# Kernel tuning notes

Measured on AMD Instinct MI355X. Metric: run time of the kernel, lower is better.

## Reference

```python
import jax, jax.numpy as jnp
import numpy as np

N = 16384

def setup_inputs() -> dict:
    key = jax.random.key(0)
    k1, k2, k3 = jax.random.split(key, 3)
    risk = jax.random.normal(k1, (N,), dtype=jnp.float32)
    time = jax.random.uniform(k2, (N,), dtype=jnp.float32)
    event = jax.random.randint(k3, (N,), 0, 2).astype(jnp.float32)
    return {"risk": risk, "time": time, "event": event}

def reference(risk, time, event):
    theta = risk.reshape(-1)  # [n]
    # Risk-set mask: R[i, j] = 1.0 iff time[j] >= time[i]  (same as the torch double loop)
    R_mat = (time[None, :] >= time[:, None]).astype(theta.dtype)  # [n, n]
    exp_theta = jnp.exp(theta)  # [n]
    log_risk_set = jnp.log(R_mat @ exp_theta)  # [n]
    loss = -((theta - log_risk_set) * event).sum() / event.sum()
    return loss
```

## Files before the change

kernel.cpp:

```cpp
#include <hip/hip_runtime.h>

#define NR    16
#define LOCB  1024
#define CAP   1536
#define BLK   1024

__device__ __forceinline__ int keyof(float t) {
    int k = (int)(t * 16384.f);
    return k < 0 ? 0 : (k > 16383 ? 16383 : k);
}

__global__ __launch_bounds__(BLK)
void cox_one(const float* __restrict__ risk,
             const float* __restrict__ tm,
             const float* __restrict__ event,
             float* __restrict__ out, int n) {
    __shared__ float4 S4[CAP];
    __shared__ int    cnt[LOCB];
    __shared__ int    off[LOCB];
    __shared__ float  bsm[LOCB];
    __shared__ float2 TE[CAP];
    __shared__ float  wsc[16], wsc2[16], sn[16];
    __shared__ int    s_m;
    __shared__ float  s_gsuf, s_den;
    const int g    = blockIdx.x;
    const int tid  = threadIdx.x;
    const int lane = tid & 63;
    const int wave = tid >> 6;

    cnt[tid] = 0; bsm[tid] = 0.f;
    if (tid == 0) { s_m = 0; s_gsuf = 0.f; s_den = 0.f; }
    __syncthreads();

    const float4* tm4 = (const float4*)tm;
    const float4* rk4 = (const float4*)risk;
    const float4* ev4 = (const float4*)event;
    const int nq = n >> 2;
    float gsufp = 0.f, denp = 0.f;

    auto quad = [&](const float4 t4, const float4 r4, const float4 e4) {
        #pragma unroll
        for (int c = 0; c < 4; ++c) {
            const float t  = c == 0 ? t4.x : c == 1 ? t4.y : c == 2 ? t4.z : t4.w;
            const float rk = c == 0 ? r4.x : c == 1 ? r4.y : c == 2 ? r4.z : r4.w;
            const float ev = c == 0 ? e4.x : c == 1 ? e4.y : c == 2 ? e4.z : e4.w;
            const int   key = keyof(t);
            const int   r   = key >> 10;
            denp += ev;
            if (r >= g) {
                const float e = __expf(rk);
                if (r > g) {
                    gsufp += e;
                } else {
                    const int lbk = key & (LOCB - 1);
                    const int pos = atomicAdd(&s_m, 1);
                    S4[pos] = make_float4(t, e, rk, ev);
                    atomicAdd(&cnt[lbk], 1);
                    atomicAdd(&bsm[lbk], e);
                }
            }
        }
    };

    if (nq == 4 * BLK) {
        float4 T[4], R[4], E[4];
        #pragma unroll
        for (int it = 0; it < 4; ++it) {
            const int q = tid + it * BLK;
            T[it] = tm4[q]; R[it] = rk4[q]; E[it] = ev4[q];
        }
        #pragma unroll
        for (int it = 0; it < 4; ++it) quad(T[it], R[it], E[it]);
    } else {
        for (int q = tid; q < nq; q += BLK) quad(tm4[q], rk4[q], ev4[q]);
    }

    #pragma unroll
    for (int o = 32; o > 0; o >>= 1) {
        denp  += __shfl_down(denp, o);
        gsufp += __shfl_down(gsufp, o);
    }
    if (lane == 0) { atomicAdd(&s_den, denp); atomicAdd(&s_gsuf, gsufp); }
    __syncthreads();
    const int   m    = s_m;
    const float gsuf = s_gsuf;
    const float den  = s_den;

    {
        const int   c = cnt[tid];
        const float e = bsm[tid];
        int incl = c;
        #pragma unroll
        for (int o = 1; o < 64; o <<= 1) {
            const int tmp = __shfl_up(incl, o);
            if (lane >= o) incl += tmp;
        }
        float fincl = e;
        #pragma unroll
        for (int o = 1; o < 64; o <<= 1) {
            const float tmp = __shfl_down(fincl, o);
            if (lane + o < 64) fincl += tmp;
        }
        if (lane == 63) wsc[wave]  = (float)incl;
        if (lane == 0)  wsc2[wave] = fincl;
        __syncthreads();
        int croff = 0;
        for (int w = 0; w < wave; ++w) croff += (int)wsc[w];
        float crsuf = 0.f;
        for (int w = wave + 1; w < 16; ++w) crsuf += wsc2[w];
        off[tid] = croff + incl - c;
        bsm[tid] = crsuf + (fincl - e);
    }
    __syncthreads();

    for (int idx = tid; idx < m; idx += BLK) {
        const float4 v   = S4[idx];
        const int    lbk = keyof(v.x) & (LOCB - 1);
        const int    pos = atomicAdd(&off[lbk], 1);
        TE[pos] = make_float2(v.x, v.y);
    }
    __syncthreads();

    float num = 0.f;
    for (int idx = tid; idx < m; idx += BLK) {
        const float4 v     = S4[idx];
        const int    b     = keyof(v.x) & (LOCB - 1);
        const int    end   = off[b];
        const int    start = end - cnt[b];
        float corr = 0.f;
        for (int q = start; q < end; ++q) {
            const float2 te = TE[q];
            corr += (te.x >= v.x) ? te.y : 0.f;
        }
        num += (v.z - logf(gsuf + bsm[b] + corr)) * v.w;
    }

    #pragma unroll
    for (int o = 32; o > 0; o >>= 1) num += __shfl_down(num, o);
    if (lane == 0) sn[wave] = num;
    __syncthreads();
    if (tid == 0) {
        float tn = 0.f;
        #pragma unroll
        for (int w = 0; w < 16; ++w) tn += sn[w];
        atomicAdd(out, -tn / den);
    }
}

extern "C" void kernel_launch(void* const* d_in, const int* in_sizes, int n_in,
                              void* d_out, int out_size, void* d_ws, size_t ws_size,
                              hipStream_t stream) {
    const float* risk  = (const float*)d_in[0];
    const float* tm    = (const float*)d_in[1];
    const float* event = (const float*)d_in[2];
    float* out = (float*)d_out;
    const int n = in_sizes[0];

    cox_one<<<NR, BLK, 0, stream>>>(risk, tm, event, out, n);
}
```

Before: 63.85 us.

## Split Cox loss into a 64-block scatter pass and a 16-block solve pass

Adds a first kernel with 64 blocks that reads each input element once, computes exp, and scatters records into per-range, per-chunk staging buffers in workspace along with per-chunk counts, exp sums and event sums. The second kernel then has each of the 16 range blocks load only its own staged records plus the small count/sum arrays, replacing the old scheme where every block rescanned all N inputs. The aim is to spread the input pass across more CUs and cut redundant global reads and exp work. The cost is an extra kernel launch and a global round trip through workspace. The old single kernel remains as a fallback when n differs.

```diff
diff --git a/kernel.cpp b/kernel.cpp
--- a/kernel.cpp
+++ b/kernel.cpp
@@ -4,22 +4,70 @@
 #define LOCB  1024
 #define CAP   1536
 #define BLK   1024
+#define NB1   64
+#define B1T   256
+#define CHCAP 256
 
 __device__ __forceinline__ int keyof(float t) {
     int k = (int)(t * 16384.f);
     return k < 0 ? 0 : (k > 16383 ? 16383 : k);
 }
 
+
+
+__global__ __launch_bounds__(B1T)
+void cox_scatter(const float* __restrict__ risk, const float* __restrict__ tm,
+                 const float* __restrict__ event, float4* __restrict__ staged,
+                 int* __restrict__ cnts, float* __restrict__ sums,
+                 float* __restrict__ denw) {
+    __shared__ int   c16[NR];
+    __shared__ float s16[NR];
+    __shared__ float sden[B1T / 64];
+    const int b = blockIdx.x, tid = threadIdx.x;
+    if (tid < NR) { c16[tid] = 0; s16[tid] = 0.f; }
+    __syncthreads();
+
+    const int   i  = b * B1T + tid;
+    const float t  = tm[i];
+    const float rk = risk[i];
+    const float ev = event[i];
+    const int   key = keyof(t);
+    const int   r   = key >> 10;
+    const float e   = __expf(rk);
+    const int   pos = atomicAdd(&c16[r], 1);
+    staged[(r * NB1 + b) * CHCAP + pos] = make_float4(t, e, rk, ev);
+    atomicAdd(&s16[r], e);
+
+    float dp = ev;
+    #pragma unroll
+    for (int o = 32; o > 0; o >>= 1) dp += __shfl_down(dp, o);
+    const int lane = tid & 63, wv = tid >> 6;
+    if (lane == 0) sden[wv] = dp;
+    __syncthreads();
+
+    if (tid < NR) {
+        cnts[tid * NB1 + b] = c16[tid];
+        sums[tid * NB1 + b] = s16[tid];
+    }
+    if (tid == 0) {
+        float d = 0.f;
+        #pragma unroll
+        for (int w = 0; w < B1T / 64; ++w) d += sden[w];
+        denw[b] = d;
+    }
+}
+
 __global__ __launch_bounds__(BLK)
-void cox_one(const float* __restrict__ risk,
-             const float* __restrict__ tm,
-             const float* __restrict__ event,
-             float* __restrict__ out, int n) {
+void cox_solve(const float4* __restrict__ staged, const int* __restrict__ cnts,
+               const float* __restrict__ sums, const float* __restrict__ denw,
+               float* __restrict__ out) {
     __shared__ float4 S4[CAP];
     __shared__ int    cnt[LOCB];
     __shared__ int    off[LOCB];
     __shared__ float  bsm[LOCB];
     __shared__ float2 TE[CAP];
+    __shared__ int    chofs[NB1];
+    __shared__ int    chcnt[NB1];
     __shared__ float  wsc[16], wsc2[16], sn[16];
     __shared__ int    s_m;
     __shared__ float  s_gsuf, s_den;
@@ -29,62 +77,50 @@
     const int wave = tid >> 6;
 
     cnt[tid] = 0; bsm[tid] = 0.f;
-    if (tid == 0) { s_m = 0; s_gsuf = 0.f; s_den = 0.f; }
-    __syncthreads();
-
-    const float4* tm4 = (const float4*)tm;
-    const float4* rk4 = (const float4*)risk;
-    const float4* ev4 = (const float4*)event;
-    const int nq = n >> 2;
-    float gsufp = 0.f, denp = 0.f;
-
-    auto quad = [&](const float4 t4, const float4 r4, const float4 e4) {
-        #pragma unroll
-        for (int c = 0; c < 4; ++c) {
-            const float t  = c == 0 ? t4.x : c == 1 ? t4.y : c == 2 ? t4.z : t4.w;
-            const float rk = c == 0 ? r4.x : c == 1 ? r4.y : c == 2 ? r4.z : r4.w;
-            const float ev = c == 0 ? e4.x : c == 1 ? e4.y : c == 2 ? e4.z : e4.w;
-            const int   key = keyof(t);
-            const int   r   = key >> 10;
-            denp += ev;
-            if (r >= g) {
-                const float e = __expf(rk);
-                if (r > g) {
-                    gsufp += e;
-                } else {
-                    const int lbk = key & (LOCB - 1);
-                    const int pos = atomicAdd(&s_m, 1);
-                    S4[pos] = make_float4(t, e, rk, ev);
-                    atomicAdd(&cnt[lbk], 1);
-                    atomicAdd(&bsm[lbk], e);
-                }
-            }
-        }
-    };
-
-    if (nq == 4 * BLK) {
-        float4 T[4], R[4], E[4];
-        #pragma unroll
-        for (int it = 0; it < 4; ++it) {
-            const int q = tid + it * BLK;
-            T[it] = tm4[q]; R[it] = rk4[q]; E[it] = ev4[q];
-        }
-        #pragma unroll
-        for (int it = 0; it < 4; ++it) quad(T[it], R[it], E[it]);
-    } else {
-        for (int q = tid; q < nq; q += BLK) quad(tm4[q], rk4[q], ev4[q]);
-    }
-
-    #pragma unroll
-    for (int o = 32; o > 0; o >>= 1) {
-        denp  += __shfl_down(denp, o);
-        gsufp += __shfl_down(gsufp, o);
-    }
-    if (lane == 0) { atomicAdd(&s_den, denp); atomicAdd(&s_gsuf, gsufp); }
+    if (tid == 0) { s_gsuf = 0.f; s_den = 0.f; }
+    __syncthreads();
+
+    if (wave == 0) {
+        const int c = cnts[g * NB1 + lane];
+        int incl = c;
+        #pragma unroll
+        for (int o = 1; o < 64; o <<= 1) {
+            const int tmp = __shfl_up(incl, o);
+            if (lane >= o) incl += tmp;
+        }
+        chofs[lane] = incl - c;
+        chcnt[lane] = c;
+        if (lane == 63) s_m = incl;
+    }
+    {
+        const int r = tid >> 6;
+        float v = (r > g) ? sums[tid] : 0.f;
+        float d = (tid < NB1) ? denw[tid] : 0.f;
+        #pragma unroll
+        for (int o = 32; o > 0; o >>= 1) {
+            v += __shfl_down(v, o);
+            d += __shfl_down(d, o);
+        }
+        if (lane == 0) { atomicAdd(&s_gsuf, v); atomicAdd(&s_den, d); }
+    }
     __syncthreads();
     const int   m    = s_m;
     const float gsuf = s_gsuf;
     const float den  = s_den;
+
+    for (int b = wave; b < NB1; b += 16) {
+        const int c  = chcnt[b];
+        const int o0 = chofs[b];
+        const float4* __restrict__ src = &staged[(g * NB1 + b) * CHCAP];
+        for (int j = lane; j < c; j += 64) {
+            const float4 v = src[j];
+            S4[o0 + j] = v;
+            const int lbk = keyof(v.x) & (LOCB - 1);
+            atomicAdd(&cnt[lbk], 1);
+            atomicAdd(&bsm[lbk], v.y);
+        }
+    }
+    __syncthreads();
 
     {
         const int   c = cnt[tid];
@@ -147,6 +183,105 @@
     }
 }
 
+__global__ __launch_bounds__(BLK)
+void cox_one(const float* __restrict__ risk, const float* __restrict__ tm,
+             const float* __restrict__ event, float* __restrict__ out, int n) {
+    __shared__ float4 S4[CAP];
+    __shared__ int    cnt[LOCB];
+    __shared__ int    off[LOCB];
+    __shared__ float  bsm[LOCB];
+    __shared__ float2 TE[CAP];
+    __shared__ float  wsc[16], wsc2[16], sn[16];
+    __shared__ int    s_m;
+    __shared__ float  s_gsuf, s_den;
+    const int g = blockIdx.x, tid = threadIdx.x;
+    const int lane = tid & 63, wave = tid >> 6;
+
+    cnt[tid] = 0; bsm[tid] = 0.f;
+    if (tid == 0) { s_m = 0; s_gsuf = 0.f; s_den = 0.f; }
+    __syncthreads();
+
+    const float4* tm4 = (const float4*)tm;
+    const float4* rk4 = (const float4*)risk;
+    const float4* ev4 = (const float4*)event;
+    const int nq = n >> 2;
+    float gsufp = 0.f, denp = 0.f;
+    for (int q = tid; q < nq; q += BLK) {
+        const float4 t4 = tm4[q], r4 = rk4[q], e4 = ev4[q];
+        #pragma unroll
+        for (int c = 0; c < 4; ++c) {
+            const float t  = c == 0 ? t4.x : c == 1 ? t4.y : c == 2 ? t4.z : t4.w;
+            const float rk = c == 0 ? r4.x : c == 1 ? r4.y : c == 2 ? r4.z : r4.w;
+            const float ev = c == 0 ? e4.x : c == 1 ? e4.y : c == 2 ? e4.z : e4.w;
+            const int key = keyof(t), r = key >> 10;
+            denp += ev;
+            if (r >= g) {
+                const float e = __expf(rk);
+                if (r > g) gsufp += e;
+                else {
+                    const int lbk = key & (LOCB - 1);
+                    const int pos = atomicAdd(&s_m, 1);
+                    S4[pos] = make_float4(t, e, rk, ev);
+                    atomicAdd(&cnt[lbk], 1);
+                    atomicAdd(&bsm[lbk], e);
+                }
+            }
+        }
+    }
+    #pragma unroll
+    for (int o = 32; o > 0; o >>= 1) { denp += __shfl_down(denp, o); gsufp += __shfl_down(gsufp, o); }
+    if (lane == 0) { atomicAdd(&s_den, denp); atomicAdd(&s_gsuf, gsufp); }
+    __syncthreads();
+    const int m = s_m; const float gsuf = s_gsuf, den = s_den;
+
+    {
+        const int c = cnt[tid]; const float e = bsm[tid];
+        int incl = c;
+        #pragma unroll
+        for (int o = 1; o < 64; o <<= 1) { const int t2 = __shfl_up(incl, o); if (lane >= o) incl += t2; }
+        float fincl = e;
+        #pragma unroll
+        for (int o = 1; o < 64; o <<= 1) { const float t2 = __shfl_down(fincl, o); if (lane + o < 64) fincl += t2; }
+        if (lane == 63) wsc[wave] = (float)incl;
+        if (lane == 0)  wsc2[wave] = fincl;
+        __syncthreads();
+        int croff = 0; for (int w = 0; w < wave; ++w) croff += (int)wsc[w];
+        float crsuf = 0.f; for (int w = wave + 1; w < 16; ++w) crsuf += wsc2[w];
+        off[tid] = croff + incl - c;
+        bsm[tid] = crsuf + (fincl - e);
+    }
+    __syncthreads();
+
+    for (int idx = tid; idx < m; idx += BLK) {
+        const float4 v = S4[idx];
+        const int lbk = keyof(v.x) & (LOCB - 1);
+        const int pos = atomicAdd(&off[lbk], 1);
+        TE[pos] = make_float2(v.x, v.y);
+    }
+    __syncthreads();
+
+    float num = 0.f;
+    for (int idx = tid; idx < m; idx += BLK) {
+        const float4 v = S4[idx];
+        const int b = keyof(v.x) & (LOCB - 1);
+        const int end = off[b], start = end - cnt[b];
+        const float t = v.x;
+        float corr = 0.f;
+        for (int q = start; q < end; ++q) { const float2 te = TE[q]; corr += (te.x >= t) ? te.y : 0.f; }
+        num += (v.z - logf(gsuf + bsm[b] + corr)) * v.w;
+    }
+    #pragma unroll
+    for (int o = 32; o > 0; o >>= 1) num += __shfl_down(num, o);
+    if (lane == 0) sn[wave] = num;
+    __syncthreads();
+    if (tid == 0) {
+        float tn = 0.f;
+        #pragma unroll
+        for (int w = 0; w < 16; ++w) tn += sn[w];
+        atomicAdd(out, -tn / den);
+    }
+}
+
 extern "C" void kernel_launch(void* const* d_in, const int* in_sizes, int n_in,
                               void* d_out, int out_size, void* d_ws, size_t ws_size,
                               hipStream_t stream) {
@@ -156,5 +291,15 @@
     float* out = (float*)d_out;
     const int n = in_sizes[0];
 
-    cox_one<<<NR, BLK, 0, stream>>>(risk, tm, event, out, n);
-}
+    if (n == NB1 * B1T) {
+        char* ws = (char*)d_ws;
+        float4* staged = (float4*)(ws);
+        int*    cnts   = (int*)  (ws + 4194304);
+        float*  sums   = (float*)(ws + 4198400);
+        float*  denw   = (float*)(ws + 4202496);
+        cox_scatter<<<NB1, B1T, 0, stream>>>(risk, tm, event, staged, cnts, sums, denw);
+        cox_solve<<<NR, BLK, 0, stream>>>(staged, cnts, sums, denw, out);
+    } else {
+        cox_one<<<NR, BLK, 0, stream>>>(risk, tm, event, out, n);
+    }
+}
```

New measurement: 64.74 us. About the same (+1.4%).
